# Kernel optimization log

Measured on AMD Instinct MI355X. Metric: run time of the kernel, lower is better.

Reference implementation:

```python
import jax, jax.numpy as jnp
import numpy as np

D = 256          # input_dim == layer_size
L = 2            # n_hidden_layers in ResLinear
B, S = 8, 4096
LR = 1e-3        # AdamW learning_rate
WD = 1e-2        # weight_decay
MAX_ALR = 0.1    # max adaptive lr
EPS = 1e-8       # AdamW eps


def _lmm(Ws, bs, x):
    # ResLinear: residual MLP blocks, hidden size D.
    # Ws: [L, D, D], bs: [L, D], x: [..., D]
    for i in range(L):
        x = x + jax.nn.silu(x @ Ws[i] + bs[i])
    return x


def setup_inputs() -> dict:
    key = jax.random.key(0)
    ks = jax.random.split(key, 9)
    scale = 0.05
    return {
        "x": jax.random.normal(ks[0], (B, S, D), dtype=jnp.float32),
        "Wk": jax.random.normal(ks[1], (D, D), dtype=jnp.float32) * scale,
        "Wq": jax.random.normal(ks[2], (D, D), dtype=jnp.float32) * scale,
        "Wv": jax.random.normal(ks[3], (D, D), dtype=jnp.float32) * scale,
        "Wlr": jax.random.normal(ks[4], (D, 1), dtype=jnp.float32) * scale,
        "blr": jnp.zeros((1,), dtype=jnp.float32),
        "Ws": jax.random.normal(ks[5], (L, D, D), dtype=jnp.float32) * scale,
        "bs": jnp.zeros((L, D), dtype=jnp.float32),
    }


def reference(x, Wk, Wq, Wv, Wlr, blr, Ws, bs):
    # Projections (LinearProjection: bias-free D->D linear)
    keys = x @ Wk          # [B, S, D]
    queries = x @ Wq       # [B, S, D]
    values = x @ Wv        # [B, S, D]
    # AdaptiveLR: sigmoid gate scaled to max_adaptive_lr, one scalar per token
    alr = (jax.nn.sigmoid(x @ Wlr + blr) * MAX_ALR).reshape(-1)  # [B*S]

    def loss_fn(params):
        Ws_, bs_ = params
        preds = _lmm(Ws_, bs_, keys).reshape(-1, D)
        tgt = values.reshape(-1, D)
        per_tok = jnp.mean((preds - tgt) ** 2, axis=-1)  # [B*S]
        return jnp.sum(per_tok * alr)

    gWs, gbs = jax.grad(loss_fn)((Ws, bs))

    # Single AdamW step from zero optimizer state (step=1):
    #   m_hat = g, v_hat = g^2  ->  p' = p*(1 - lr*wd) - lr * g / (|g| + eps)
    def adamw_step(p, g):
        return p * (1.0 - LR * WD) - LR * g / (jnp.sqrt(g * g) + EPS)

    nWs = adamw_step(Ws, gWs)
    nbs = adamw_step(bs, gbs)

    retrieved = _lmm(nWs, nbs, queries)  # [B, S, D]
    # surprises = -grads
    return retrieved, -gWs, -gbs
```

## Files before the change

kernel.cpp:

```cpp
#include <hip/hip_runtime.h>
#include <math.h>


#define NTOK 32768
#define NM ((size_t)NTOK * 256)
#define LRc 1e-3f
#define WDc 1e-2f
#define EPSc 1e-8f

typedef __attribute__((ext_vector_type(8))) short bf16x8;
typedef __attribute__((ext_vector_type(4))) float f32x4;

__device__ __forceinline__ float b2f(unsigned short u) {
    union { unsigned int i; float f; } c;
    c.i = ((unsigned int)u) << 16;
    return c.f;
}
__device__ __forceinline__ unsigned short f2b(float f) {
    union { float f; unsigned int i; } c;
    c.f = f;
    unsigned int i = c.i;
    return (unsigned short)((i + 0x7FFFu + ((i >> 16) & 1u)) >> 16);
}
__device__ __forceinline__ float sigm(float z) { return 1.f / (1.f + __expf(-z)); }
__device__ __forceinline__ float siluf(float z) { return z * sigm(z); }
__device__ __forceinline__ float dsiluf(float z) {
    float s = sigm(z);
    return s * (1.f + z * (1.f - s));
}
__device__ __forceinline__ void unpack4(uint2 u, float* f) {
    f[0] = b2f(u.x & 0xFFFF); f[1] = b2f(u.x >> 16);
    f[2] = b2f(u.y & 0xFFFF); f[3] = b2f(u.y >> 16);
}
__device__ __forceinline__ uint2 pack4(const float* f) {
    uint2 o;
    o.x = (unsigned)f2b(f[0]) | ((unsigned)f2b(f[1]) << 16);
    o.y = (unsigned)f2b(f[2]) | ((unsigned)f2b(f[3]) << 16);
    return o;
}

#define WSTR 264
#define SSTR 40

__global__ __launch_bounds__(512, 4) void wgemm3_k(
    const float* __restrict__ x, const float* __restrict__ Wlr,
    const float* __restrict__ blr, const unsigned short* __restrict__ wt,
    unsigned short* __restrict__ Kb, unsigned short* __restrict__ Qb,
    unsigned short* __restrict__ Vb, float* __restrict__ alr) {
    __shared__ unsigned short Ws[128 * WSTR];
    __shared__ unsigned short Sc[8][16 * SSTR];
    __shared__ float Ls[256];
    const int n0 = blockIdx.x * 128, m0 = blockIdx.y * 128;
    const int tid = threadIdx.x, lane = tid & 63, wv = tid >> 6;
    const int cc = lane & 15, q = lane >> 4;
    const int t0 = m0 + wv * 16, tok = t0 + cc;

    if (tid < 256) Ls[tid] = Wlr[tid];
    __syncthreads();

    const float* xp = x + (size_t)tok * 256 + q * 8;
    bf16x8 xf[8];
    float s = 0.f;
#pragma unroll
    for (int c = 0; c < 8; c++) {
        float xv[8];
        *(float4*)&xv[0] = *(const float4*)(xp + c * 32);
        *(float4*)&xv[4] = *(const float4*)(xp + c * 32 + 4);
        float wl[8];
        *(float4*)&wl[0] = *(const float4*)&Ls[c * 32 + q * 8];
        *(float4*)&wl[4] = *(const float4*)&Ls[c * 32 + q * 8 + 4];
        unsigned short us[8];
#pragma unroll
        for (int j = 0; j < 8; j++) {
            s += xv[j] * wl[j];
            us[j] = f2b(xv[j]);
        }
        xf[c] = *(bf16x8*)us;
    }
    s += __shfl_xor(s, 16);
    s += __shfl_xor(s, 32);
    if (n0 == 0 && q == 0) alr[tok] = 0.1f * sigm(s + blr[0]);

    unsigned short* sc = &Sc[wv][0];
    const int rtok = lane >> 2, roct = (lane & 3) * 8;
    unsigned short* const outs[3] = {Kb, Qb, Vb};

    for (int z = 0; z < 3; z++) {
        __syncthreads();
#pragma unroll
        for (int it = 0; it < 8; it++) {
            int i = it * 512 + tid;
            int row = i >> 5, g8 = i & 31;
            *(uint4*)&Ws[row * WSTR + g8 * 8] =
                *(const uint4*)(wt + (size_t)z * 65536 +
                                (size_t)(n0 + row) * 256 + g8 * 8);
        }
        __syncthreads();

        f32x4 acc[8];
#pragma unroll
        for (int t = 0; t < 8; t++) acc[t] = (f32x4){0.f, 0.f, 0.f, 0.f};
#pragma unroll
        for (int c = 0; c < 8; c++) {
#pragma unroll
            for (int nt = 0; nt < 8; nt++) {
                bf16x8 wf =
                    *(const bf16x8*)&Ws[(nt * 16 + cc) * WSTR + c * 32 + q * 8];
                acc[nt] = __builtin_amdgcn_mfma_f32_16x16x32_bf16(wf, xf[c],
                                                                  acc[nt], 0, 0, 0);
            }
        }

        unsigned short* Cb = outs[z];
#pragma unroll
        for (int pr = 0; pr < 4; pr++) {
#pragma unroll
            for (int h = 0; h < 2; h++) {
                const int nt = pr * 2 + h;
                f32x4 c4 = acc[nt];
                float o[4] = {c4[0], c4[1], c4[2], c4[3]};
                *(uint2*)&sc[cc * SSTR + h * 16 + q * 4] = pack4(o);
            }
            uint4 pk = *(const uint4*)&sc[rtok * SSTR + roct];
            *(uint4*)(Cb + (size_t)(t0 + rtok) * 256 + n0 + pr * 32 + roct) = pk;
        }
    }
}

template <int EPI>
__global__ __launch_bounds__(512, 4) void wgemm_k(
    const unsigned short* __restrict__ A, const unsigned short* __restrict__ Bt,
    const float* __restrict__ bias, const unsigned short* __restrict__ Rin,
    const unsigned short* __restrict__ Zin, const unsigned short* __restrict__ Vb,
    const float* __restrict__ alr, float* __restrict__ gB,
    unsigned short* __restrict__ Cb, float* __restrict__ Cf,
    unsigned short* __restrict__ Zout, unsigned short* __restrict__ Rout) {
    __shared__ unsigned short Ws[128 * WSTR];
    __shared__ unsigned short Sc[8][16 * SSTR];
    __shared__ float accsh[128];
    const int n0 = blockIdx.x * 128, m0 = blockIdx.y * 128;
    const int tid = threadIdx.x, lane = tid & 63, wv = tid >> 6;
    const int cc = lane & 15, q = lane >> 4;

    const int t0 = m0 + wv * 16;
    const unsigned short* xp = A + (size_t)(t0 + cc) * 256 + q * 8;
    bf16x8 xf[8];
#pragma unroll
    for (int c = 0; c < 8; c++) xf[c] = *(const bf16x8*)(xp + c * 32);

    if (EPI == 2 || EPI == 5) {
        if (tid < 128) accsh[tid] = 0.f;
    }

#pragma unroll
    for (int it = 0; it < 8; it++) {
        int i = it * 512 + tid;
        int row = i >> 5, g8 = i & 31;
        *(uint4*)&Ws[row * WSTR + g8 * 8] =
            *(const uint4*)(Bt + (size_t)(n0 + row) * 256 + g8 * 8);
    }
    __syncthreads();

    f32x4 acc[8];
#pragma unroll
    for (int t = 0; t < 8; t++) acc[t] = (f32x4){0.f, 0.f, 0.f, 0.f};

#pragma unroll
    for (int c = 0; c < 8; c++) {
#pragma unroll
        for (int nt = 0; nt < 8; nt++) {
            bf16x8 wf = *(const bf16x8*)&Ws[(nt * 16 + cc) * WSTR + c * 32 + q * 8];
            acc[nt] = __builtin_amdgcn_mfma_f32_16x16x32_bf16(wf, xf[c],
                                                              acc[nt], 0, 0, 0);
        }
    }

    const int tok = t0 + cc;
    float lalr = 0.f;
    if (EPI == 5) lalr = alr[tok] * (2.f / 256.f);
    unsigned short* sc = &Sc[wv][0];
    const int rtok = lane >> 2, roct = (lane & 3) * 8;

#pragma unroll
    for (int pr = 0; pr < 4; pr++) {
        float o2[2][4], z2[2][4];
#pragma unroll
        for (int h = 0; h < 2; h++) {
            const int nt = pr * 2 + h;
            const int gcol = n0 + nt * 16 + q * 4;
            const size_t off = (size_t)tok * 256 + gcol;
            f32x4 c = acc[nt];
            float v[4] = {c[0], c[1], c[2], c[3]};
            if (EPI == 1) {
                float bv[4], a[4];
                *(float4*)bv = *(const float4*)(bias + gcol);
                unpack4(*(const uint2*)(A + off), a);
#pragma unroll
                for (int r = 0; r < 4; r++) {
                    float z = v[r] + bv[r];
                    z2[h][r] = z;
                    o2[h][r] = a[r] + siluf(z);
                }
            } else if (EPI == 5) {
                float bv[4], a[4], vv[4];
                *(float4*)bv = *(const float4*)(bias + gcol);
                unpack4(*(const uint2*)(A + off), a);
                unpack4(*(const uint2*)(Vb + off), vv);
#pragma unroll
                for (int r = 0; r < 4; r++) {
                    float z = v[r] + bv[r];
                    float h2 = a[r] + siluf(z);
                    float dh = lalr * (h2 - vv[r]);
                    o2[h][r] = dh * dsiluf(z);
                    z2[h][r] = dh;
                }
            } else if (EPI == 2) {
                float ri[4], zi[4];
                unpack4(*(const uint2*)(Rin + off), ri);
                unpack4(*(const uint2*)(Zin + off), zi);
#pragma unroll
                for (int r = 0; r < 4; r++)
                    o2[h][r] = (v[r] + ri[r]) * dsiluf(zi[r]);
            } else {
                float bv[4], a[4];
                *(float4*)bv = *(const float4*)(bias + gcol);
                unpack4(*(const uint2*)(A + off), a);
#pragma unroll
                for (int r = 0; r < 4; r++) o2[h][r] = a[r] + siluf(v[r] + bv[r]);
            }
            if (EPI == 4) {
                *(float4*)(Cf + off) = *(float4*)o2[h];
            }
            if (EPI == 2 || EPI == 5) {
                float s0 = o2[h][0], s1 = o2[h][1], s2 = o2[h][2], s3 = o2[h][3];
#pragma unroll
                for (int m = 1; m < 16; m <<= 1) {
                    s0 += __shfl_xor(s0, m);
                    s1 += __shfl_xor(s1, m);
                    s2 += __shfl_xor(s2, m);
                    s3 += __shfl_xor(s3, m);
                }
                if (cc == 0) {
                    const int lc = nt * 16 + q * 4;
                    atomicAdd(&accsh[lc], s0);
                    atomicAdd(&accsh[lc + 1], s1);
                    atomicAdd(&accsh[lc + 2], s2);
                    atomicAdd(&accsh[lc + 3], s3);
                }
            }
        }
        if (EPI == 4) continue;
#pragma unroll
        for (int h = 0; h < 2; h++)
            *(uint2*)&sc[cc * SSTR + h * 16 + q * 4] = pack4(o2[h]);
        uint4 pk = *(const uint4*)&sc[rtok * SSTR + roct];
        *(uint4*)(Cb + (size_t)(t0 + rtok) * 256 + n0 + pr * 32 + roct) = pk;
        if (EPI == 1 || EPI == 5) {
#pragma unroll
            for (int h = 0; h < 2; h++)
                *(uint2*)&sc[cc * SSTR + h * 16 + q * 4] = pack4(z2[h]);
            uint4 pk2 = *(const uint4*)&sc[rtok * SSTR + roct];
            unsigned short* P2 = (EPI == 1) ? Zout : Rout;
            *(uint4*)(P2 + (size_t)(t0 + rtok) * 256 + n0 + pr * 32 + roct) = pk2;
        }
    }
    if (EPI == 2 || EPI == 5) {
        __syncthreads();
        if (tid < 128) atomicAdd(&gB[n0 + tid], accsh[tid]);
    }
}

__global__ __launch_bounds__(512, 4) void rgemm_k(
    const unsigned short* __restrict__ Kb, const unsigned short* __restrict__ h1b,
    const unsigned short* __restrict__ dz0b,
    const unsigned short* __restrict__ dz1b, float* __restrict__ pbuf) {
    __shared__ unsigned short As[128 * 64];
    __shared__ unsigned short Bs2[128 * 64];
    const int z = blockIdx.z, layer = z >> 5, zc = z & 31;
    const unsigned short* Ag = layer ? h1b : Kb;
    const unsigned short* Bg = layer ? dz1b : dz0b;
    const int t0 = zc * 1024;
    const int j0 = blockIdx.x * 128, i0 = blockIdx.y * 128;
    const int tid = threadIdx.x, lane = tid & 63, wave = tid >> 6;

    const int half = tid >> 8;
    const int t9 = tid & 255;
    const int ptq = t9 >> 4;
    const int pi = (t9 & 15) * 8;
    const unsigned short* sg = half ? Bg : Ag;
    const int nb = half ? j0 : i0;
    unsigned int* dst = (unsigned int*)(half ? Bs2 : As);
    const unsigned short* gp = sg + (size_t)(t0 + ptq * 2) * 256 + nb + pi;

    const int wr = (wave >> 2) * 64, wc = (wave & 3) * 32;
    const int fr = lane & 15, fkb = lane >> 4;

    f32x4 acc[4][2];
#pragma unroll
    for (int i = 0; i < 4; i++)
#pragma unroll
        for (int j = 0; j < 2; j++) acc[i][j] = (f32x4){0.f, 0.f, 0.f, 0.f};

    uint4 u0 = *(const uint4*)gp;
    uint4 u1 = *(const uint4*)(gp + 256);
    gp += 32 * 256;

    for (int it = 0; it < 32; it++) {
        const unsigned int* w0 = (const unsigned int*)&u0;
        const unsigned int* w1 = (const unsigned int*)&u1;
#pragma unroll
        for (int ii = 0; ii < 8; ii++) {
            unsigned int lo = (w0[ii >> 1] >> (16 * (ii & 1))) & 0xFFFFu;
            unsigned int hi = (w1[ii >> 1] >> (16 * (ii & 1))) & 0xFFFFu;
            const int col = pi + ii;
            const int s2 = ((col >> 3) ^ col) & 3;
            const int s4 = ((col >> 2) ^ (col >> 5)) & 1;
            dst[col * 32 + (ptq ^ (s2 << 2) ^ (s4 << 4))] = lo | (hi << 16);
        }
        __syncthreads();
        if (it < 31) {
            u0 = *(const uint4*)gp;
            u1 = *(const uint4*)(gp + 256);
            gp += 32 * 256;
        }
        bf16x8 af[4], bfr[2];
#pragma unroll
        for (int i = 0; i < 4; i++) {
            const int col = wr + i * 16 + fr;
            const int s2 = ((col >> 3) ^ col) & 3;
            const int s4 = ((col >> 2) ^ (col >> 5)) & 1;
            af[i] = *(const bf16x8*)&As[col * 64 + (fkb ^ s2 ^ (s4 << 2)) * 8];
        }
#pragma unroll
        for (int j = 0; j < 2; j++) {
            const int col = wc + j * 16 + fr;
            const int s2 = ((col >> 3) ^ col) & 3;
            const int s4 = ((col >> 2) ^ (col >> 5)) & 1;
            bfr[j] = *(const bf16x8*)&Bs2[col * 64 + (fkb ^ s2 ^ (s4 << 2)) * 8];
        }
#pragma unroll
        for (int i = 0; i < 4; i++)
#pragma unroll
            for (int j = 0; j < 2; j++)
                acc[i][j] = __builtin_amdgcn_mfma_f32_16x16x32_bf16(
                    af[i], bfr[j], acc[i][j], 0, 0, 0);
        __syncthreads();
    }

    float* P = pbuf + (size_t)((layer << 5) + zc) * 65536;
    const int r0 = fkb * 4;
#pragma unroll
    for (int mi = 0; mi < 4; mi++)
#pragma unroll
        for (int ni = 0; ni < 2; ni++) {
            f32x4 c = acc[mi][ni];
#pragma unroll
            for (int r = 0; r < 4; r++)
                P[(size_t)(i0 + wr + mi * 16 + r0 + r) * 256 +
                  (j0 + wc + ni * 16 + fr)] = c[r];
        }
}

__global__ __launch_bounds__(256) void gradstep_k(
    const float* __restrict__ pbuf, const float* __restrict__ Ws,
    const float* __restrict__ bs, const float* __restrict__ accB,
    unsigned short* __restrict__ nWt, float* __restrict__ nb,
    float* __restrict__ outSW, float* __restrict__ outSb) {
    const int bi = blockIdx.x;
    if (bi < 512) {
        const int idx = bi * 256 + threadIdx.x;
        const int layer = idx >> 16, rc = idx & 65535;
        const float* p = pbuf + (size_t)layer * 32 * 65536 + rc;
        float g = 0.f;
#pragma unroll 8
        for (int c = 0; c < 32; c++) g += p[(size_t)c * 65536];
        outSW[idx] = -g;
        float nw = Ws[idx] * (1.f - LRc * WDc) - LRc * g / (fabsf(g) + EPSc);
        const int l = idx >> 16, k = (idx >> 8) & 255, n = idx & 255;
        nWt[(size_t)l * 65536 + n * 256 + k] = f2b(nw);
    } else {
        for (int i = threadIdx.x; i < 512; i += 256) {
            float g = accB[i];
            outSb[i] = -g;
            nb[i] = bs[i] * (1.f - LRc * WDc) - LRc * g / (fabsf(g) + EPSc);
        }
    }
}

__global__ __launch_bounds__(256) void prep_w_k(
    const float* __restrict__ Wk, const float* __restrict__ Wq,
    const float* __restrict__ Wv, const float* __restrict__ Ws,
    unsigned short* __restrict__ wt, float* __restrict__ accB) {
    const int bi = blockIdx.x;
    if (bi < 1536) {
        const int z = bi >> 8;
        const int idx = (bi & 255) * 256 + threadIdx.x;
        const float* src = z == 0 ? Wk : z == 1 ? Wq : z == 2 ? Wv
                         : z == 3 ? Ws : Ws + 65536;
        unsigned short* dst = wt + (size_t)z * 65536;
        float v = src[idx];
        if (z == 5)
            dst[idx] = f2b(v);
        else
            dst[(idx & 255) * 256 + (idx >> 8)] = f2b(v);
    } else {
        accB[threadIdx.x] = 0.f;
        accB[threadIdx.x + 256] = 0.f;
    }
}

extern "C" void kernel_launch(void* const* d_in, const int* in_sizes, int n_in,
                              void* d_out, int out_size, void* d_ws,
                              size_t ws_size, hipStream_t stream) {
    const float* x = (const float*)d_in[0];
    const float* Wk = (const float*)d_in[1];
    const float* Wq = (const float*)d_in[2];
    const float* Wv = (const float*)d_in[3];
    const float* Wlr = (const float*)d_in[4];
    const float* blr = (const float*)d_in[5];
    const float* Ws = (const float*)d_in[6];
    const float* bs = (const float*)d_in[7];

    unsigned short* S = (unsigned short*)d_ws;
    unsigned short* xb = S + 0 * NM;
    unsigned short* Kb = S + 1 * NM;
    unsigned short* Qb = S + 2 * NM;
    unsigned short* Vb = S + 3 * NM;
    unsigned short* z0b = S + 4 * NM;
    unsigned short* h1b = S + 5 * NM;
    unsigned short* dz1b = S + 6 * NM;
    unsigned short* dh2b = S + 7 * NM;
    unsigned short* dz0b = S + 8 * NM;
    float* pbuf = (float*)(S + 9 * NM);
    unsigned short* r1b = xb;

    unsigned short* wt = S + 11 * NM;
    unsigned short* W0t = wt + 3 * 65536;
    unsigned short* W1t = wt + 4 * 65536;
    unsigned short* W1b = wt + 5 * 65536;
    unsigned short* nW0t = wt + 6 * 65536;
    unsigned short* nW1t = wt + 7 * 65536;
    float* ft = (float*)(wt + 8 * 65536);
    float* alr = ft;
    float* accB = ft + 32768;
    float* nb = accB + 512;

    float* out_ret = (float*)d_out;
    float* out_sW = out_ret + NM;
    float* out_sb = out_sW + 131072;

    dim3 blk5(512);
    dim3 blk(256);
    dim3 g_tall(2, 256);

    prep_w_k<<<1537, blk, 0, stream>>>(Wk, Wq, Wv, Ws, wt, accB);

    wgemm3_k<<<g_tall, blk5, 0, stream>>>(x, Wlr, blr, wt, Kb, Qb, Vb, alr);

    wgemm_k<1><<<g_tall, blk5, 0, stream>>>(Kb, W0t, bs, nullptr, nullptr,
                                            nullptr, nullptr, nullptr, h1b,
                                            nullptr, z0b, nullptr);

    wgemm_k<5><<<g_tall, blk5, 0, stream>>>(h1b, W1t, bs + 256, nullptr,
                                            nullptr, Vb, alr, accB + 256,
                                            dz1b, nullptr, nullptr, dh2b);

    wgemm_k<2><<<g_tall, blk5, 0, stream>>>(dz1b, W1b, nullptr, dh2b, z0b,
                                            nullptr, nullptr, accB, dz0b,
                                            nullptr, nullptr, nullptr);

    rgemm_k<<<dim3(2, 2, 64), blk5, 0, stream>>>(Kb, h1b, dz0b, dz1b, pbuf);

    gradstep_k<<<513, blk, 0, stream>>>(pbuf, Ws, bs, accB, nW0t, nb, out_sW,
                                        out_sb);

    wgemm_k<3><<<g_tall, blk5, 0, stream>>>(Qb, nW0t, nb, nullptr, nullptr,
                                            nullptr, nullptr, nullptr, r1b,
                                            nullptr, nullptr, nullptr);
    wgemm_k<4><<<g_tall, blk5, 0, stream>>>(r1b, nW1t, nb + 256, nullptr,
                                            nullptr, nullptr, nullptr, nullptr,
                                            nullptr, out_ret, nullptr, nullptr);
}
```

Before: 247.7 us.

## Load weight tiles via global_load_lds with XOR-swizzled pre-permuted layout

Weight tiles are now copied straight from global memory into LDS with the global_load_lds builtin, which skips the round trip through registers. To keep the MFMA operand reads free of bank conflicts without padding rows, the prep and gradstep kernels write the bf16 weights in an XOR-swizzled column order. The LDS reads apply the matching swizzle. The per-tile weight load is small next to the MFMA work, so the effect on the total may be modest, and any mismatch in the swizzle or in the LDS destination layout used by the builtin would corrupt results.

```diff
diff --git a/kernel.cpp b/kernel.cpp
--- a/kernel.cpp
+++ b/kernel.cpp
@@ -39,16 +39,43 @@
     return o;
 }
 
-#define WSTR 264
+__device__ __forceinline__ void gload16(const unsigned short* g,
+                                        unsigned short* l) {
+#if __has_builtin(__builtin_amdgcn_global_load_lds)
+    __builtin_amdgcn_global_load_lds(
+        (const __attribute__((address_space(1))) unsigned int*)g,
+        (__attribute__((address_space(3))) unsigned int*)l, 16, 0, 0);
+#else
+    *(uint4*)l = *(const uint4*)g;
+#endif
+}
+
+__device__ __forceinline__ int pswz(int row, int col) {
+    return (col & 7) | (((col >> 3) ^ (row & 7)) << 3);
+}
+
 #define SSTR 40
+
+#define FILLW(SRC)                                                         \
+    {                                                                      \
+        _Pragma("unroll") for (int it_ = 0; it_ < 8; it_++) {              \
+            const int L_ = it_ * 512 + tid;                                \
+            gload16((SRC) + (size_t)L_ * 8,                                \
+                    &Ws[(size_t)(it_ * 512 + wv * 64) * 8]);               \
+        }                                                                  \
+    }
+
+#define WREAD(nt_, c_)                                        \
+    (*(const bf16x8*)&Ws[((nt_)*16 + cc) * 256 +              \
+                         ((((c_)*4 + q) ^ (cc & 7)) << 3)])
 
 __global__ __launch_bounds__(512, 4) void wgemm3_k(
     const float* __restrict__ x, const float* __restrict__ Wlr,
     const float* __restrict__ blr, const unsigned short* __restrict__ wt,
     unsigned short* __restrict__ Kb, unsigned short* __restrict__ Qb,
     unsigned short* __restrict__ Vb, float* __restrict__ alr) {
-    __shared__ unsigned short Ws[128 * WSTR];
-    __shared__ unsigned short Sc[8][16 * SSTR];
+    __shared__ __attribute__((aligned(16))) unsigned short Ws[128 * 256];
+    __shared__ __attribute__((aligned(16))) unsigned short Sc[8][16 * SSTR];
     __shared__ float Ls[256];
     const int n0 = blockIdx.x * 128, m0 = blockIdx.y * 128;
     const int tid = threadIdx.x, lane = tid & 63, wv = tid >> 6;
@@ -87,14 +114,7 @@
 
     for (int z = 0; z < 3; z++) {
         __syncthreads();
-#pragma unroll
-        for (int it = 0; it < 8; it++) {
-            int i = it * 512 + tid;
-            int row = i >> 5, g8 = i & 31;
-            *(uint4*)&Ws[row * WSTR + g8 * 8] =
-                *(const uint4*)(wt + (size_t)z * 65536 +
-                                (size_t)(n0 + row) * 256 + g8 * 8);
-        }
+        FILLW(wt + (size_t)z * 65536 + (size_t)n0 * 256);
         __syncthreads();
 
         f32x4 acc[8];
@@ -104,8 +124,7 @@
         for (int c = 0; c < 8; c++) {
 #pragma unroll
             for (int nt = 0; nt < 8; nt++) {
-                bf16x8 wf =
-                    *(const bf16x8*)&Ws[(nt * 16 + cc) * WSTR + c * 32 + q * 8];
+                bf16x8 wf = WREAD(nt, c);
                 acc[nt] = __builtin_amdgcn_mfma_f32_16x16x32_bf16(wf, xf[c],
                                                                   acc[nt], 0, 0, 0);
             }
@@ -135,8 +154,8 @@
     const float* __restrict__ alr, float* __restrict__ gB,
     unsigned short* __restrict__ Cb, float* __restrict__ Cf,
     unsigned short* __restrict__ Zout, unsigned short* __restrict__ Rout) {
-    __shared__ unsigned short Ws[128 * WSTR];
-    __shared__ unsigned short Sc[8][16 * SSTR];
+    __shared__ __attribute__((aligned(16))) unsigned short Ws[128 * 256];
+    __shared__ __attribute__((aligned(16))) unsigned short Sc[8][16 * SSTR];
     __shared__ float accsh[128];
     const int n0 = blockIdx.x * 128, m0 = blockIdx.y * 128;
     const int tid = threadIdx.x, lane = tid & 63, wv = tid >> 6;
@@ -152,13 +171,7 @@
         if (tid < 128) accsh[tid] = 0.f;
     }
 
-#pragma unroll
-    for (int it = 0; it < 8; it++) {
-        int i = it * 512 + tid;
-        int row = i >> 5, g8 = i & 31;
-        *(uint4*)&Ws[row * WSTR + g8 * 8] =
-            *(const uint4*)(Bt + (size_t)(n0 + row) * 256 + g8 * 8);
-    }
+    FILLW(Bt + (size_t)n0 * 256);
     __syncthreads();
 
     f32x4 acc[8];
@@ -169,7 +182,7 @@
     for (int c = 0; c < 8; c++) {
 #pragma unroll
         for (int nt = 0; nt < 8; nt++) {
-            bf16x8 wf = *(const bf16x8*)&Ws[(nt * 16 + cc) * WSTR + c * 32 + q * 8];
+            bf16x8 wf = WREAD(nt, c);
             acc[nt] = __builtin_amdgcn_mfma_f32_16x16x32_bf16(wf, xf[c],
                                                               acc[nt], 0, 0, 0);
         }
@@ -377,7 +390,7 @@
         outSW[idx] = -g;
         float nw = Ws[idx] * (1.f - LRc * WDc) - LRc * g / (fabsf(g) + EPSc);
         const int l = idx >> 16, k = (idx >> 8) & 255, n = idx & 255;
-        nWt[(size_t)l * 65536 + n * 256 + k] = f2b(nw);
+        nWt[(size_t)l * 65536 + n * 256 + pswz(n, k)] = f2b(nw);
     } else {
         for (int i = threadIdx.x; i < 512; i += 256) {
             float g = accB[i];
@@ -399,10 +412,10 @@
                          : z == 3 ? Ws : Ws + 65536;
         unsigned short* dst = wt + (size_t)z * 65536;
         float v = src[idx];
-        if (z == 5)
-            dst[idx] = f2b(v);
-        else
-            dst[(idx & 255) * 256 + (idx >> 8)] = f2b(v);
+        int row, col;
+        if (z == 5) { row = idx >> 8; col = idx & 255; }
+        else        { row = idx & 255; col = idx >> 8; }
+        dst[row * 256 + pswz(row, col)] = f2b(v);
     } else {
         accB[threadIdx.x] = 0.f;
         accB[threadIdx.x + 256] = 0.f;
```

New measurement: 252.3 us. About the same (+1.9%).
